# Optimization experiments

Measured on AMD Instinct MI355X. Metric: run time of the kernel, lower is better.

The kernel has to match this reference:

```python
import math
import jax, jax.numpy as jnp
import numpy as np

K, B, T = 6, 8, 12
DIM = 256
DH = 64          # dim_head
NH = 8           # num_heads
G = 8            # offset_groups
INNER = DH * NH  # 512
HALF = INNER // 2  # 256
OFF_D = INNER // G  # 64
HBEV = WBEV = 256
PW = PH = 102.4   # x/y range extents
SCALE = DH ** -0.5
OFF_SCALE = 4.0


def setup_inputs() -> dict:
    key = jax.random.key(0)
    ks = jax.random.split(key, 20)
    w = lambda i, shape: jax.random.normal(ks[i], shape, jnp.float32) * 0.05
    return {
        "dec_embed": jax.random.normal(ks[0], (K, B, T, DIM), jnp.float32),
        "bev_feat": jax.random.normal(ks[1], (B, DIM, HBEV, WBEV), jnp.float32),
        "query_scale": jax.random.uniform(ks[2], (K, B, T, HALF), jnp.float32),
        "ref_points": (jax.random.uniform(ks[3], (K, B, T, 2), jnp.float32) * 2.0 - 1.0) * 51.2,
        "Wq": w(4, (DIM, HALF)), "bq": jnp.zeros((HALF,), jnp.float32),
        "Wk": w(5, (DIM, HALF)),
        "Wv": w(6, (DIM, HALF)),
        "pq_W1": w(7, (HALF, HALF)), "pq_b1": jnp.zeros((HALF,), jnp.float32),
        "pq_W2": w(8, (HALF, HALF)), "pq_b2": jnp.zeros((HALF,), jnp.float32),
        "pk_W1": w(9, (HALF, HALF)), "pk_b1": jnp.zeros((HALF,), jnp.float32),
        "pk_W2": w(10, (HALF, HALF)), "pk_b2": jnp.zeros((HALF,), jnp.float32),
        "off_W1": w(11, (OFF_D // 2, OFF_D)), "off_b1": jnp.zeros((OFF_D,), jnp.float32),
        "off_W2": w(12, (OFF_D, 2)), "off_b2": jnp.zeros((2,), jnp.float32),
        "out_W": w(13, (HALF, DIM)), "out_b": jnp.zeros((DIM,), jnp.float32),
    }


def _grid_sample(im, grid):
    """F.grid_sample, bilinear, padding_mode='zeros', align_corners=False.
    im: (B,C,H,W), grid: (B,Hg,Wg,2) with (x,y) in [-1,1]. Returns (B,C,Hg,Wg)."""
    Bn, C, Hh, Ww = im.shape
    gx, gy = grid[..., 0], grid[..., 1]
    ix = ((gx + 1.0) * Ww - 1.0) * 0.5
    iy = ((gy + 1.0) * Hh - 1.0) * 0.5
    ix0 = jnp.floor(ix)
    iy0 = jnp.floor(iy)
    wx = (ix - ix0)[:, None]  # (B,1,Hg,Wg)
    wy = (iy - iy0)[:, None]
    imf = im.reshape(Bn, C, Hh * Ww)

    def gather(xq, yq):
        valid = (xq >= 0) & (xq < Ww) & (yq >= 0) & (yq < Hh)
        idx = (jnp.clip(yq, 0, Hh - 1) * Ww + jnp.clip(xq, 0, Ww - 1)).astype(jnp.int32)
        v = jnp.take_along_axis(imf, idx.reshape(Bn, 1, -1), axis=2)
        v = v.reshape(Bn, C, *xq.shape[1:])
        return v * valid[:, None].astype(im.dtype)

    v00 = gather(ix0, iy0)
    v01 = gather(ix0 + 1, iy0)
    v10 = gather(ix0, iy0 + 1)
    v11 = gather(ix0 + 1, iy0 + 1)
    return (v00 * (1 - wx) * (1 - wy) + v01 * wx * (1 - wy)
            + v10 * (1 - wx) * wy + v11 * wx * wy)


def _sine_embed(pos, hidden=256, temp=40.0):
    """DAB-DETR style sine embedding for 2D positions. pos: (...,2) -> (...,hidden)."""
    half = hidden // 2
    dim_t = jnp.arange(half, dtype=pos.dtype)
    dim_t = temp ** (2.0 * jnp.floor(dim_t / 2.0) / half)
    sc = 2.0 * math.pi
    ex = pos[..., 0, None] * sc / dim_t
    ey = pos[..., 1, None] * sc / dim_t

    def interleave(e):
        return jnp.stack((jnp.sin(e[..., 0::2]), jnp.cos(e[..., 1::2])), axis=-1).reshape(*e.shape[:-1], -1)

    return jnp.concatenate((interleave(ey), interleave(ex)), axis=-1)


def reference(dec_embed, bev_feat, query_scale, ref_points,
              Wq, bq, Wk, Wv,
              pq_W1, pq_b1, pq_W2, pq_b2,
              pk_W1, pk_b1, pk_W2, pk_b2,
              off_W1, off_b1, off_W2, off_b2,
              out_W, out_b):
    de = dec_embed.transpose(1, 0, 2, 3)     # (B,K,T,D)
    qs = query_scale.transpose(1, 0, 2, 3)   # (B,K,T,256)
    rp = ref_points.transpose(1, 0, 2, 3)    # (B,K,T,2)
    Bn, Kn, Tn = de.shape[:3]

    con_q = de @ Wq + bq                                    # (B,K,T,256)
    oin = con_q.reshape(Bn, Kn, Tn, G, OFF_D // 2)          # (B,K,T,G,32)
    off = jax.nn.gelu(oin @ off_W1 + off_b1, approximate=False)
    off = jnp.tanh(off @ off_W2 + off_b2) * OFF_SCALE       # (B,K,T,G,2)

    vgrid = rp[..., None, :] + off                          # (B,K,T,G,2)
    vgrid = vgrid.reshape(Bn, Kn * Tn, G, 2)
    norm = jnp.array([2.0 / PW, 2.0 / PH], vgrid.dtype)
    vgrid_scaled = vgrid * norm                             # ref_from_Q normalization

    con_k_map = jnp.einsum('bchw,cd->bdhw', bev_feat, Wk)   # 1x1 conv, no bias
    v_map = jnp.einsum('bchw,cd->bdhw', bev_feat, Wv)
    con_k = _grid_sample(con_k_map, vgrid_scaled)           # (B,256,KT,G)
    v = _grid_sample(v_map, vgrid_scaled)                   # (B,256,KT,G)

    ref_scaled = rp * norm                                  # (B,K,T,2)
    qse = _sine_embed(ref_scaled)                           # (B,K,T,256)
    pos_q = (jax.nn.relu(qse @ pq_W1 + pq_b1) @ pq_W2 + pq_b2) * qs
    kse = _sine_embed(vgrid_scaled)                         # (B,KT,G,256)
    pos_k = jax.nn.relu(kse @ pk_W1 + pk_b1) @ pk_W2 + pk_b2

    BS = Bn * Kn * Tn
    dh = HALF // NH  # 32 per-head content dim
    cq = con_q.reshape(BS, 1, NH, dh)
    pq = pos_q.reshape(BS, 1, NH, dh)
    ck = con_k.transpose(0, 2, 3, 1).reshape(BS, G, NH, dh)
    pk = pos_k.reshape(BS, G, NH, dh)
    vv = v.transpose(0, 2, 3, 1).reshape(BS, G, NH, dh)

    q = jnp.concatenate([cq, pq], -1).transpose(0, 2, 1, 3) * SCALE  # (BS,NH,1,64)
    k = jnp.concatenate([ck, pk], -1).transpose(0, 2, 1, 3)          # (BS,NH,G,64)
    vv = vv.transpose(0, 2, 1, 3)                                    # (BS,NH,G,32)

    sim = jnp.einsum('bhid,bhjd->bhij', q, k)               # (BS,NH,1,G)
    attn = jax.nn.softmax(sim, axis=-1)
    out = jnp.einsum('bhij,bhjd->bhid', attn, vv)           # (BS,NH,1,32)

    out = out.transpose(0, 2, 1, 3).reshape(Bn, Kn, Tn, HALF).transpose(1, 0, 2, 3)
    out = out @ out_W + out_b                               # (K,B,T,D)
    return dec_embed + out
```

## Files before the change

kernel.cpp:

```cpp
#include <hip/hip_runtime.h>
#include <math.h>

#define NK 6
#define NB 8
#define NT 12
#define D 256
#define DP (D+4)
#define NG 8
#define NHD 8
#define HW 256
#define NQ (NK*NB*NT)

__global__ __launch_bounds__(256)
void dca_kernel(const float* __restrict__ dec_embed,
                const float* __restrict__ bev_feat,
                const float* __restrict__ query_scale,
                const float* __restrict__ ref_points,
                const float* __restrict__ Wq,     const float* __restrict__ bq,
                const float* __restrict__ Wk,     const float* __restrict__ Wv,
                const float* __restrict__ pq_W1,  const float* __restrict__ pq_b1,
                const float* __restrict__ pq_W2,  const float* __restrict__ pq_b2,
                const float* __restrict__ pk_W1,  const float* __restrict__ pk_b1,
                const float* __restrict__ pk_W2,  const float* __restrict__ pk_b2,
                const float* __restrict__ off_W1, const float* __restrict__ off_b1,
                const float* __restrict__ off_W2, const float* __restrict__ off_b2,
                const float* __restrict__ out_W,  const float* __restrict__ out_b,
                float* __restrict__ out)
{
    __shared__ float de[D];
    __shared__ float conq[D];
    __shared__ float qse[D];
    __shared__ float tmp1[D];
    __shared__ float posq[D];
    __shared__ float oatt[D];
    __shared__ float h1[NG][64];
    __shared__ float gxy[NG][2];
    __shared__ float sim[NHD][NG];
    __shared__ float psum[64][4];
    __shared__ float samp[NG][DP];
    __shared__ float kseW[NG][DP];
    __shared__ float tmpk[NG][DP];
    __shared__ float wqk [NHD][DP];
    __shared__ float wqpk[NHD][DP];

    const int tid = threadIdx.x;
    const int q   = blockIdx.x;
    const int bb  = (q / NT) % NB;

    const float NORM = 0.01953125f;
    const float TWO_PI = 6.28318530717958647692f;
    const float L2_40_OVER_64 = 5.32192809488736234787f / 64.0f;

    de[tid] = dec_embed[(size_t)q * D + tid];
    __syncthreads();

    {
        float acc = bq[tid];
        #pragma unroll 4
        for (int i = 0; i < D; i += 4) {
            float4 d4 = *(const float4*)&de[i];
            acc += d4.x * Wq[(i + 0) * D + tid];
            acc += d4.y * Wq[(i + 1) * D + tid];
            acc += d4.z * Wq[(i + 2) * D + tid];
            acc += d4.w * Wq[(i + 3) * D + tid];
        }
        conq[tid] = acc;
        float rx = ref_points[(size_t)q * 2 + 0] * NORM;
        float ry = ref_points[(size_t)q * 2 + 1] * NORM;
        float pos = (tid < 128) ? ry : rx;
        int m = (tid & 127) >> 1;
        float freq = TWO_PI / exp2f((float)m * L2_40_OVER_64);
        float e = pos * freq;
        qse[tid] = (tid & 1) ? __cosf(e) : __sinf(e);
    }
    __syncthreads();

    for (int idx = tid; idx < NG * 64; idx += 256) {
        int g = idx >> 6, j = idx & 63;
        float acc = off_b1[j];
        #pragma unroll
        for (int i = 0; i < 32; i += 4) {
            float4 c4 = *(const float4*)&conq[g * 32 + i];
            acc += c4.x * off_W1[(i + 0) * 64 + j];
            acc += c4.y * off_W1[(i + 1) * 64 + j];
            acc += c4.z * off_W1[(i + 2) * 64 + j];
            acc += c4.w * off_W1[(i + 3) * 64 + j];
        }
        h1[g][j] = 0.5f * acc * (1.0f + erff(acc * 0.70710678118654752440f));
    }
    __syncthreads();

    if (tid < NG * 2) {
        int g = tid >> 1, c = tid & 1;
        float acc = off_b2[c];
        #pragma unroll
        for (int j = 0; j < 64; j += 4) {
            float4 hh = *(const float4*)&h1[g][j];
            acc += hh.x * off_W2[(j + 0) * 2 + c];
            acc += hh.y * off_W2[(j + 1) * 2 + c];
            acc += hh.z * off_W2[(j + 2) * 2 + c];
            acc += hh.w * off_W2[(j + 3) * 2 + c];
        }
        float off = tanhf(acc) * 4.0f;
        float rp  = ref_points[(size_t)q * 2 + c];
        gxy[g][c] = (rp + off) * NORM;
    }
    __syncthreads();

    {
        const float* ch = bev_feat + ((size_t)bb * D + tid) * HW * HW;
        float v00[NG], v01[NG], v10[NG], v11[NG], wxA[NG], wyA[NG];
        #pragma unroll
        for (int g = 0; g < NG; ++g) {
            float gx = gxy[g][0], gy = gxy[g][1];
            float ix = ((gx + 1.0f) * HW - 1.0f) * 0.5f;
            float iy = ((gy + 1.0f) * HW - 1.0f) * 0.5f;
            float fx0 = floorf(ix), fy0 = floorf(iy);
            wxA[g] = ix - fx0; wyA[g] = iy - fy0;
            int x0 = (int)fx0, y0 = (int)fy0;
            bool xin0 = (x0 >= 0) && (x0 < HW);
            bool xin1 = (x0 + 1 >= 0) && (x0 + 1 < HW);
            bool yin0 = (y0 >= 0) && (y0 < HW);
            bool yin1 = (y0 + 1 >= 0) && (y0 + 1 < HW);
            v00[g] = (yin0 && xin0) ? ch[y0 * HW + x0]           : 0.f;
            v01[g] = (yin0 && xin1) ? ch[y0 * HW + x0 + 1]       : 0.f;
            v10[g] = (yin1 && xin0) ? ch[(y0 + 1) * HW + x0]     : 0.f;
            v11[g] = (yin1 && xin1) ? ch[(y0 + 1) * HW + x0 + 1] : 0.f;
        }
        {
            int m = (tid & 127) >> 1;
            float freq = TWO_PI / exp2f((float)m * L2_40_OVER_64);
            #pragma unroll
            for (int g = 0; g < NG; ++g) {
                float pos = (tid < 128) ? gxy[g][1] : gxy[g][0];
                float e = pos * freq;
                kseW[g][tid] = (tid & 1) ? __cosf(e) : __sinf(e);
            }
        }
        {
            float acc[NHD] = {0.f,0.f,0.f,0.f,0.f,0.f,0.f,0.f};
            const float* wkrow = Wk + (size_t)tid * D;
            #pragma unroll
            for (int c = 0; c < D; c += 4) {
                float4 w  = *(const float4*)&wkrow[c];
                float4 cq = *(const float4*)&conq[c];
                acc[c >> 5] += w.x * cq.x + w.y * cq.y + w.z * cq.z + w.w * cq.w;
            }
            #pragma unroll
            for (int h = 0; h < NHD; ++h) wqk[h][tid] = acc[h];
        }
        #pragma unroll
        for (int g = 0; g < NG; ++g) {
            float wx = wxA[g], wy = wyA[g];
            samp[g][tid] = v00[g] * (1.f - wx) * (1.f - wy) + v01[g] * wx * (1.f - wy)
                         + v10[g] * (1.f - wx) * wy         + v11[g] * wx * wy;
        }
    }
    __syncthreads();

    {
        float acc[NG + 1];
        float biask = pk_b1[tid];
        #pragma unroll
        for (int g = 0; g < NG; ++g) acc[g] = biask;
        acc[NG] = pq_b1[tid];
        #pragma unroll 2
        for (int i = 0; i < D; i += 4) {
            float k0 = pk_W1[(i + 0) * D + tid], k1 = pk_W1[(i + 1) * D + tid];
            float k2 = pk_W1[(i + 2) * D + tid], k3 = pk_W1[(i + 3) * D + tid];
            float q0 = pq_W1[(i + 0) * D + tid], q1 = pq_W1[(i + 1) * D + tid];
            float q2 = pq_W1[(i + 2) * D + tid], q3 = pq_W1[(i + 3) * D + tid];
            #pragma unroll
            for (int g = 0; g < NG; ++g) {
                float4 s = *(const float4*)&kseW[g][i];
                acc[g] += s.x * k0 + s.y * k1 + s.z * k2 + s.w * k3;
            }
            float4 t = *(const float4*)&qse[i];
            acc[NG] += t.x * q0 + t.y * q1 + t.z * q2 + t.w * q3;
        }
        #pragma unroll
        for (int g = 0; g < NG; ++g) tmpk[g][tid] = fmaxf(acc[g], 0.f);
        tmp1[tid] = fmaxf(acc[NG], 0.f);
    }
    __syncthreads();

    {
        float a2 = pq_b2[tid];
        #pragma unroll 4
        for (int i = 0; i < D; i += 4) {
            float4 t = *(const float4*)&tmp1[i];
            a2 += t.x * pq_W2[(i + 0) * D + tid];
            a2 += t.y * pq_W2[(i + 1) * D + tid];
            a2 += t.z * pq_W2[(i + 2) * D + tid];
            a2 += t.w * pq_W2[(i + 3) * D + tid];
        }
        posq[tid] = a2 * query_scale[(size_t)q * D + tid];
    }
    __syncthreads();

    {
        float acc[NHD] = {0.f,0.f,0.f,0.f,0.f,0.f,0.f,0.f};
        const float* wrow = pk_W2 + (size_t)tid * D;
        #pragma unroll
        for (int c = 0; c < D; c += 4) {
            float4 w  = *(const float4*)&wrow[c];
            float4 p4 = *(const float4*)&posq[c];
            acc[c >> 5] += w.x * p4.x + w.y * p4.y + w.z * p4.z + w.w * p4.w;
        }
        #pragma unroll
        for (int h = 0; h < NHD; ++h) wqpk[h][tid] = acc[h];
    }
    __syncthreads();

    {
        int pair = tid >> 2, part = tid & 3;
        int h = pair >> 3, g = pair & 7;
        int i0 = part * 64;
        float s = 0.f;
        #pragma unroll
        for (int i = i0; i < i0 + 64; i += 4) {
            float4 a = *(const float4*)&samp[g][i];
            float4 b = *(const float4*)&wqk[h][i];
            float4 c = *(const float4*)&tmpk[g][i];
            float4 d = *(const float4*)&wqpk[h][i];
            s += a.x * b.x + a.y * b.y + a.z * b.z + a.w * b.w;
            s += c.x * d.x + c.y * d.y + c.z * d.z + c.w * d.w;
        }
        psum[pair][part] = s;
    }
    __syncthreads();
    if (tid < 64) {
        float s = psum[tid][0] + psum[tid][1] + psum[tid][2] + psum[tid][3];
        sim[tid >> 3][tid & 7] = s * 0.125f;
    }
    __syncthreads();

    if (tid < NHD) {
        int h = tid;
        float mx = sim[h][0];
        for (int g = 1; g < NG; ++g) mx = fmaxf(mx, sim[h][g]);
        float ex[NG], sum = 0.f;
        #pragma unroll
        for (int g = 0; g < NG; ++g) { ex[g] = __expf(sim[h][g] - mx); sum += ex[g]; }
        float inv = 1.0f / sum;
        #pragma unroll
        for (int g = 0; g < NG; ++g) sim[h][g] = ex[g] * inv;
    }
    __syncthreads();

    {
        float wsm[NHD];
        #pragma unroll
        for (int h = 0; h < NHD; ++h) wsm[h] = 0.f;
        #pragma unroll
        for (int g = 0; g < NG; ++g) {
            float sv = samp[g][tid];
            #pragma unroll
            for (int h = 0; h < NHD; ++h) wsm[h] += sim[h][g] * sv;
        }
        #pragma unroll
        for (int h = 0; h < NHD; ++h) kseW[h][tid] = wsm[h];
    }
    __syncthreads();

    {
        int h = tid >> 5;
        float acc = 0.f;
        #pragma unroll 4
        for (int i = 0; i < D; i += 4) {
            float4 w4 = *(const float4*)&kseW[h][i];
            acc += w4.x * Wv[(i + 0) * D + tid];
            acc += w4.y * Wv[(i + 1) * D + tid];
            acc += w4.z * Wv[(i + 2) * D + tid];
            acc += w4.w * Wv[(i + 3) * D + tid];
        }
        oatt[tid] = acc;
    }
    __syncthreads();

    {
        float acc = out_b[tid];
        #pragma unroll 4
        for (int i = 0; i < D; i += 4) {
            float4 o4 = *(const float4*)&oatt[i];
            acc += o4.x * out_W[(i + 0) * D + tid];
            acc += o4.y * out_W[(i + 1) * D + tid];
            acc += o4.z * out_W[(i + 2) * D + tid];
            acc += o4.w * out_W[(i + 3) * D + tid];
        }
        out[(size_t)q * D + tid] = acc + de[tid];
    }
}

extern "C" void kernel_launch(void* const* d_in, const int* in_sizes, int n_in,
                              void* d_out, int out_size, void* d_ws, size_t ws_size,
                              hipStream_t stream) {
    const float* dec_embed   = (const float*)d_in[0];
    const float* bev_feat    = (const float*)d_in[1];
    const float* query_scale = (const float*)d_in[2];
    const float* ref_points  = (const float*)d_in[3];
    const float* Wq     = (const float*)d_in[4];
    const float* bq     = (const float*)d_in[5];
    const float* Wk     = (const float*)d_in[6];
    const float* Wv     = (const float*)d_in[7];
    const float* pq_W1  = (const float*)d_in[8];
    const float* pq_b1  = (const float*)d_in[9];
    const float* pq_W2  = (const float*)d_in[10];
    const float* pq_b2  = (const float*)d_in[11];
    const float* pk_W1  = (const float*)d_in[12];
    const float* pk_b1  = (const float*)d_in[13];
    const float* pk_W2  = (const float*)d_in[14];
    const float* pk_b2  = (const float*)d_in[15];
    const float* off_W1 = (const float*)d_in[16];
    const float* off_b1 = (const float*)d_in[17];
    const float* off_W2 = (const float*)d_in[18];
    const float* off_b2 = (const float*)d_in[19];
    const float* out_W  = (const float*)d_in[20];
    const float* out_b  = (const float*)d_in[21];
    float* out = (float*)d_out;

    dca_kernel<<<NQ, 256, 0, stream>>>(dec_embed, bev_feat, query_scale, ref_points,
                                       Wq, bq, Wk, Wv,
                                       pq_W1, pq_b1, pq_W2, pq_b2,
                                       pk_W1, pk_b1, pk_W2, pk_b2,
                                       off_W1, off_b1, off_W2, off_b2,
                                       out_W, out_b, out);
}
```

Measured before the change: 722.5 us.

## Process two queries per block to reuse weight loads across queries

Each block now handles a pair of queries instead of one, halving the grid to 288 blocks. Every weight matrix (Wq, Wk, pk/pq MLPs, Wv, out_W) is loaded once per block and applied to both queries, halving global weight traffic per query. In exchange, shared memory roughly doubles, register pressure rises (e.g. 18 accumulators in the positional MLP), and a 288-block grid may underfill the 256 CUs on MI355X.

```diff
diff --git a/kernel.cpp b/kernel.cpp
--- a/kernel.cpp
+++ b/kernel.cpp
@@ -10,285 +10,319 @@
 #define NHD 8
 #define HW 256
 #define NQ (NK*NB*NT)
+#define NBLK (NQ/2)
 
 __global__ __launch_bounds__(256)
-void dca_kernel(const float* __restrict__ dec_embed,
-                const float* __restrict__ bev_feat,
-                const float* __restrict__ query_scale,
-                const float* __restrict__ ref_points,
-                const float* __restrict__ Wq,     const float* __restrict__ bq,
-                const float* __restrict__ Wk,     const float* __restrict__ Wv,
-                const float* __restrict__ pq_W1,  const float* __restrict__ pq_b1,
-                const float* __restrict__ pq_W2,  const float* __restrict__ pq_b2,
-                const float* __restrict__ pk_W1,  const float* __restrict__ pk_b1,
-                const float* __restrict__ pk_W2,  const float* __restrict__ pk_b2,
-                const float* __restrict__ off_W1, const float* __restrict__ off_b1,
-                const float* __restrict__ off_W2, const float* __restrict__ off_b2,
-                const float* __restrict__ out_W,  const float* __restrict__ out_b,
-                float* __restrict__ out)
+void dca_pair(const float* __restrict__ dec_embed,
+              const float* __restrict__ bev_feat,
+              const float* __restrict__ query_scale,
+              const float* __restrict__ ref_points,
+              const float* __restrict__ Wq,     const float* __restrict__ bq,
+              const float* __restrict__ Wk,     const float* __restrict__ Wv,
+              const float* __restrict__ pq_W1,  const float* __restrict__ pq_b1,
+              const float* __restrict__ pq_W2,  const float* __restrict__ pq_b2,
+              const float* __restrict__ pk_W1,  const float* __restrict__ pk_b1,
+              const float* __restrict__ pk_W2,  const float* __restrict__ pk_b2,
+              const float* __restrict__ off_W1, const float* __restrict__ off_b1,
+              const float* __restrict__ off_W2, const float* __restrict__ off_b2,
+              const float* __restrict__ out_W,  const float* __restrict__ out_b,
+              float* __restrict__ out)
 {
-    __shared__ float de[D];
-    __shared__ float conq[D];
-    __shared__ float qse[D];
-    __shared__ float tmp1[D];
-    __shared__ float posq[D];
-    __shared__ float oatt[D];
-    __shared__ float h1[NG][64];
-    __shared__ float gxy[NG][2];
-    __shared__ float sim[NHD][NG];
-    __shared__ float psum[64][4];
-    __shared__ float samp[NG][DP];
-    __shared__ float kseW[NG][DP];
-    __shared__ float tmpk[NG][DP];
-    __shared__ float wqk [NHD][DP];
-    __shared__ float wqpk[NHD][DP];
+    __shared__ float de[2][D];
+    __shared__ float conq[2][D];
+    __shared__ float qse[2][D];
+    __shared__ float posq[2][D];
+    __shared__ float h1buf[2][NG*64];
+    __shared__ float gxy[2][NG][2];
+    __shared__ float sim[2][NHD][NG];
+    __shared__ float samp[2][NG][DP];
+    __shared__ float kst [2][NG][DP];
+    __shared__ float wqk [2][NHD][DP];
+    __shared__ float wqpk[2][NHD][DP];
 
     const int tid = threadIdx.x;
-    const int q   = blockIdx.x;
-    const int bb  = (q / NT) % NB;
+    const int q0  = blockIdx.x * 2;
+    const int bb  = (q0 / NT) % NB;
 
     const float NORM = 0.01953125f;
     const float TWO_PI = 6.28318530717958647692f;
     const float L2_40_OVER_64 = 5.32192809488736234787f / 64.0f;
 
-    de[tid] = dec_embed[(size_t)q * D + tid];
-    __syncthreads();
-
-    {
-        float acc = bq[tid];
+    de[0][tid] = dec_embed[(size_t)q0 * D + tid];
+    de[1][tid] = dec_embed[(size_t)(q0 + 1) * D + tid];
+    __syncthreads();
+
+    {
+        float a0 = bq[tid], a1 = a0;
         #pragma unroll 4
         for (int i = 0; i < D; i += 4) {
-            float4 d4 = *(const float4*)&de[i];
-            acc += d4.x * Wq[(i + 0) * D + tid];
-            acc += d4.y * Wq[(i + 1) * D + tid];
-            acc += d4.z * Wq[(i + 2) * D + tid];
-            acc += d4.w * Wq[(i + 3) * D + tid];
-        }
-        conq[tid] = acc;
-        float rx = ref_points[(size_t)q * 2 + 0] * NORM;
-        float ry = ref_points[(size_t)q * 2 + 1] * NORM;
-        float pos = (tid < 128) ? ry : rx;
+            float w0 = Wq[(i + 0) * D + tid], w1 = Wq[(i + 1) * D + tid];
+            float w2 = Wq[(i + 2) * D + tid], w3 = Wq[(i + 3) * D + tid];
+            float4 d0 = *(const float4*)&de[0][i];
+            float4 d1 = *(const float4*)&de[1][i];
+            a0 += d0.x * w0 + d0.y * w1 + d0.z * w2 + d0.w * w3;
+            a1 += d1.x * w0 + d1.y * w1 + d1.z * w2 + d1.w * w3;
+        }
+        conq[0][tid] = a0;
+        conq[1][tid] = a1;
         int m = (tid & 127) >> 1;
         float freq = TWO_PI / exp2f((float)m * L2_40_OVER_64);
-        float e = pos * freq;
-        qse[tid] = (tid & 1) ? __cosf(e) : __sinf(e);
+        #pragma unroll
+        for (int p = 0; p < 2; ++p) {
+            float rx = ref_points[(size_t)(q0 + p) * 2 + 0] * NORM;
+            float ry = ref_points[(size_t)(q0 + p) * 2 + 1] * NORM;
+            float pos = (tid < 128) ? ry : rx;
+            float e = pos * freq;
+            qse[p][tid] = (tid & 1) ? __cosf(e) : __sinf(e);
+        }
     }
     __syncthreads();
 
     for (int idx = tid; idx < NG * 64; idx += 256) {
         int g = idx >> 6, j = idx & 63;
-        float acc = off_b1[j];
+        float a0 = off_b1[j], a1 = a0;
         #pragma unroll
         for (int i = 0; i < 32; i += 4) {
-            float4 c4 = *(const float4*)&conq[g * 32 + i];
-            acc += c4.x * off_W1[(i + 0) * 64 + j];
-            acc += c4.y * off_W1[(i + 1) * 64 + j];
-            acc += c4.z * off_W1[(i + 2) * 64 + j];
-            acc += c4.w * off_W1[(i + 3) * 64 + j];
-        }
-        h1[g][j] = 0.5f * acc * (1.0f + erff(acc * 0.70710678118654752440f));
+            float w0 = off_W1[(i + 0) * 64 + j], w1 = off_W1[(i + 1) * 64 + j];
+            float w2 = off_W1[(i + 2) * 64 + j], w3 = off_W1[(i + 3) * 64 + j];
+            float4 c0 = *(const float4*)&conq[0][g * 32 + i];
+            float4 c1 = *(const float4*)&conq[1][g * 32 + i];
+            a0 += c0.x * w0 + c0.y * w1 + c0.z * w2 + c0.w * w3;
+            a1 += c1.x * w0 + c1.y * w1 + c1.z * w2 + c1.w * w3;
+        }
+        h1buf[0][idx] = 0.5f * a0 * (1.0f + erff(a0 * 0.70710678118654752440f));
+        h1buf[1][idx] = 0.5f * a1 * (1.0f + erff(a1 * 0.70710678118654752440f));
     }
     __syncthreads();
 
     if (tid < NG * 2) {
         int g = tid >> 1, c = tid & 1;
-        float acc = off_b2[c];
+        float a0 = off_b2[c], a1 = a0;
         #pragma unroll
         for (int j = 0; j < 64; j += 4) {
-            float4 hh = *(const float4*)&h1[g][j];
-            acc += hh.x * off_W2[(j + 0) * 2 + c];
-            acc += hh.y * off_W2[(j + 1) * 2 + c];
-            acc += hh.z * off_W2[(j + 2) * 2 + c];
-            acc += hh.w * off_W2[(j + 3) * 2 + c];
-        }
-        float off = tanhf(acc) * 4.0f;
-        float rp  = ref_points[(size_t)q * 2 + c];
-        gxy[g][c] = (rp + off) * NORM;
-    }
-    __syncthreads();
-
-    {
-        const float* ch = bev_feat + ((size_t)bb * D + tid) * HW * HW;
-        float v00[NG], v01[NG], v10[NG], v11[NG], wxA[NG], wyA[NG];
-        #pragma unroll
-        for (int g = 0; g < NG; ++g) {
-            float gx = gxy[g][0], gy = gxy[g][1];
-            float ix = ((gx + 1.0f) * HW - 1.0f) * 0.5f;
-            float iy = ((gy + 1.0f) * HW - 1.0f) * 0.5f;
-            float fx0 = floorf(ix), fy0 = floorf(iy);
-            wxA[g] = ix - fx0; wyA[g] = iy - fy0;
-            int x0 = (int)fx0, y0 = (int)fy0;
-            bool xin0 = (x0 >= 0) && (x0 < HW);
-            bool xin1 = (x0 + 1 >= 0) && (x0 + 1 < HW);
-            bool yin0 = (y0 >= 0) && (y0 < HW);
-            bool yin1 = (y0 + 1 >= 0) && (y0 + 1 < HW);
-            v00[g] = (yin0 && xin0) ? ch[y0 * HW + x0]           : 0.f;
-            v01[g] = (yin0 && xin1) ? ch[y0 * HW + x0 + 1]       : 0.f;
-            v10[g] = (yin1 && xin0) ? ch[(y0 + 1) * HW + x0]     : 0.f;
-            v11[g] = (yin1 && xin1) ? ch[(y0 + 1) * HW + x0 + 1] : 0.f;
+            float w0 = off_W2[(j + 0) * 2 + c], w1 = off_W2[(j + 1) * 2 + c];
+            float w2 = off_W2[(j + 2) * 2 + c], w3 = off_W2[(j + 3) * 2 + c];
+            float4 h0 = *(const float4*)&h1buf[0][g * 64 + j];
+            float4 h14 = *(const float4*)&h1buf[1][g * 64 + j];
+            a0 += h0.x * w0 + h0.y * w1 + h0.z * w2 + h0.w * w3;
+            a1 += h14.x * w0 + h14.y * w1 + h14.z * w2 + h14.w * w3;
+        }
+        gxy[0][g][c] = (ref_points[(size_t)q0 * 2 + c] + tanhf(a0) * 4.0f) * NORM;
+        gxy[1][g][c] = (ref_points[(size_t)(q0 + 1) * 2 + c] + tanhf(a1) * 4.0f) * NORM;
+    }
+    __syncthreads();
+
+    {
+        const float* ch = bev_feat + ((size_t)bb * D + tid) * (HW * HW);
+        int m = (tid & 127) >> 1;
+        float freq = TWO_PI / exp2f((float)m * L2_40_OVER_64);
+        #pragma unroll 1
+        for (int p = 0; p < 2; ++p) {
+            float v00[NG], v01[NG], v10[NG], v11[NG], wxA[NG], wyA[NG];
+            #pragma unroll
+            for (int g = 0; g < NG; ++g) {
+                float gx = gxy[p][g][0], gy = gxy[p][g][1];
+                float ix = ((gx + 1.0f) * HW - 1.0f) * 0.5f;
+                float iy = ((gy + 1.0f) * HW - 1.0f) * 0.5f;
+                float fx0 = floorf(ix), fy0 = floorf(iy);
+                wxA[g] = ix - fx0; wyA[g] = iy - fy0;
+                int x0 = (int)fx0, y0 = (int)fy0;
+                bool xin0 = (x0 >= 0) && (x0 < HW);
+                bool xin1 = (x0 + 1 >= 0) && (x0 + 1 < HW);
+                bool yin0 = (y0 >= 0) && (y0 < HW);
+                bool yin1 = (y0 + 1 >= 0) && (y0 + 1 < HW);
+                v00[g] = (yin0 && xin0) ? ch[y0 * HW + x0]           : 0.f;
+                v01[g] = (yin0 && xin1) ? ch[y0 * HW + x0 + 1]       : 0.f;
+                v10[g] = (yin1 && xin0) ? ch[(y0 + 1) * HW + x0]     : 0.f;
+                v11[g] = (yin1 && xin1) ? ch[(y0 + 1) * HW + x0 + 1] : 0.f;
+            }
+            #pragma unroll
+            for (int g = 0; g < NG; ++g) {
+                float pos = (tid < 128) ? gxy[p][g][1] : gxy[p][g][0];
+                float e = pos * freq;
+                kst[p][g][tid] = (tid & 1) ? __cosf(e) : __sinf(e);
+            }
+            #pragma unroll
+            for (int g = 0; g < NG; ++g) {
+                float wx = wxA[g], wy = wyA[g];
+                samp[p][g][tid] = v00[g] * (1.f - wx) * (1.f - wy) + v01[g] * wx * (1.f - wy)
+                                + v10[g] * (1.f - wx) * wy         + v11[g] * wx * wy;
+            }
         }
         {
-            int m = (tid & 127) >> 1;
-            float freq = TWO_PI / exp2f((float)m * L2_40_OVER_64);
-            #pragma unroll
-            for (int g = 0; g < NG; ++g) {
-                float pos = (tid < 128) ? gxy[g][1] : gxy[g][0];
-                float e = pos * freq;
-                kseW[g][tid] = (tid & 1) ? __cosf(e) : __sinf(e);
-            }
-        }
-        {
-            float acc[NHD] = {0.f,0.f,0.f,0.f,0.f,0.f,0.f,0.f};
+            float ak[2][NHD] = {{0.f}};
             const float* wkrow = Wk + (size_t)tid * D;
             #pragma unroll
             for (int c = 0; c < D; c += 4) {
                 float4 w  = *(const float4*)&wkrow[c];
-                float4 cq = *(const float4*)&conq[c];
-                acc[c >> 5] += w.x * cq.x + w.y * cq.y + w.z * cq.z + w.w * cq.w;
-            }
-            #pragma unroll
-            for (int h = 0; h < NHD; ++h) wqk[h][tid] = acc[h];
-        }
-        #pragma unroll
-        for (int g = 0; g < NG; ++g) {
-            float wx = wxA[g], wy = wyA[g];
-            samp[g][tid] = v00[g] * (1.f - wx) * (1.f - wy) + v01[g] * wx * (1.f - wy)
-                         + v10[g] * (1.f - wx) * wy         + v11[g] * wx * wy;
-        }
-    }
-    __syncthreads();
-
-    {
-        float acc[NG + 1];
-        float biask = pk_b1[tid];
-        #pragma unroll
-        for (int g = 0; g < NG; ++g) acc[g] = biask;
-        acc[NG] = pq_b1[tid];
+                float4 c0 = *(const float4*)&conq[0][c];
+                float4 c1 = *(const float4*)&conq[1][c];
+                ak[0][c >> 5] += w.x * c0.x + w.y * c0.y + w.z * c0.z + w.w * c0.w;
+                ak[1][c >> 5] += w.x * c1.x + w.y * c1.y + w.z * c1.z + w.w * c1.w;
+            }
+            #pragma unroll
+            for (int h = 0; h < NHD; ++h) {
+                wqk[0][h][tid] = ak[0][h];
+                wqk[1][h][tid] = ak[1][h];
+            }
+        }
+    }
+    __syncthreads();
+
+    {
+        float acc[2][NG + 1];
+        float bk = pk_b1[tid], bqv = pq_b1[tid];
+        #pragma unroll
+        for (int p = 0; p < 2; ++p) {
+            #pragma unroll
+            for (int g = 0; g < NG; ++g) acc[p][g] = bk;
+            acc[p][NG] = bqv;
+        }
         #pragma unroll 2
         for (int i = 0; i < D; i += 4) {
             float k0 = pk_W1[(i + 0) * D + tid], k1 = pk_W1[(i + 1) * D + tid];
             float k2 = pk_W1[(i + 2) * D + tid], k3 = pk_W1[(i + 3) * D + tid];
-            float q0 = pq_W1[(i + 0) * D + tid], q1 = pq_W1[(i + 1) * D + tid];
-            float q2 = pq_W1[(i + 2) * D + tid], q3 = pq_W1[(i + 3) * D + tid];
-            #pragma unroll
-            for (int g = 0; g < NG; ++g) {
-                float4 s = *(const float4*)&kseW[g][i];
-                acc[g] += s.x * k0 + s.y * k1 + s.z * k2 + s.w * k3;
-            }
-            float4 t = *(const float4*)&qse[i];
-            acc[NG] += t.x * q0 + t.y * q1 + t.z * q2 + t.w * q3;
-        }
-        #pragma unroll
-        for (int g = 0; g < NG; ++g) tmpk[g][tid] = fmaxf(acc[g], 0.f);
-        tmp1[tid] = fmaxf(acc[NG], 0.f);
-    }
-    __syncthreads();
-
-    {
-        float a2 = pq_b2[tid];
+            float u0 = pq_W1[(i + 0) * D + tid], u1 = pq_W1[(i + 1) * D + tid];
+            float u2 = pq_W1[(i + 2) * D + tid], u3 = pq_W1[(i + 3) * D + tid];
+            #pragma unroll
+            for (int p = 0; p < 2; ++p) {
+                #pragma unroll
+                for (int g = 0; g < NG; ++g) {
+                    float4 s = *(const float4*)&kst[p][g][i];
+                    acc[p][g] += s.x * k0 + s.y * k1 + s.z * k2 + s.w * k3;
+                }
+                float4 t = *(const float4*)&qse[p][i];
+                acc[p][NG] += t.x * u0 + t.y * u1 + t.z * u2 + t.w * u3;
+            }
+        }
+        __syncthreads();
+        #pragma unroll
+        for (int p = 0; p < 2; ++p) {
+            #pragma unroll
+            for (int g = 0; g < NG; ++g) kst[p][g][tid] = fmaxf(acc[p][g], 0.f);
+            h1buf[p][tid] = fmaxf(acc[p][NG], 0.f);
+        }
+    }
+    __syncthreads();
+
+    {
+        float a0 = pq_b2[tid], a1 = a0;
         #pragma unroll 4
         for (int i = 0; i < D; i += 4) {
-            float4 t = *(const float4*)&tmp1[i];
-            a2 += t.x * pq_W2[(i + 0) * D + tid];
-            a2 += t.y * pq_W2[(i + 1) * D + tid];
-            a2 += t.z * pq_W2[(i + 2) * D + tid];
-            a2 += t.w * pq_W2[(i + 3) * D + tid];
-        }
-        posq[tid] = a2 * query_scale[(size_t)q * D + tid];
-    }
-    __syncthreads();
-
-    {
-        float acc[NHD] = {0.f,0.f,0.f,0.f,0.f,0.f,0.f,0.f};
+            float w0 = pq_W2[(i + 0) * D + tid], w1 = pq_W2[(i + 1) * D + tid];
+            float w2 = pq_W2[(i + 2) * D + tid], w3 = pq_W2[(i + 3) * D + tid];
+            float4 t0 = *(const float4*)&h1buf[0][i];
+            float4 t1 = *(const float4*)&h1buf[1][i];
+            a0 += t0.x * w0 + t0.y * w1 + t0.z * w2 + t0.w * w3;
+            a1 += t1.x * w0 + t1.y * w1 + t1.z * w2 + t1.w * w3;
+        }
+        posq[0][tid] = a0 * query_scale[(size_t)q0 * D + tid];
+        posq[1][tid] = a1 * query_scale[(size_t)(q0 + 1) * D + tid];
+    }
+    __syncthreads();
+
+    {
+        float aw[2][NHD] = {{0.f}};
         const float* wrow = pk_W2 + (size_t)tid * D;
         #pragma unroll
         for (int c = 0; c < D; c += 4) {
             float4 w  = *(const float4*)&wrow[c];
-            float4 p4 = *(const float4*)&posq[c];
-            acc[c >> 5] += w.x * p4.x + w.y * p4.y + w.z * p4.z + w.w * p4.w;
-        }
-        #pragma unroll
-        for (int h = 0; h < NHD; ++h) wqpk[h][tid] = acc[h];
-    }
-    __syncthreads();
-
-    {
-        int pair = tid >> 2, part = tid & 3;
-        int h = pair >> 3, g = pair & 7;
-        int i0 = part * 64;
+            float4 p0 = *(const float4*)&posq[0][c];
+            float4 p1 = *(const float4*)&posq[1][c];
+            aw[0][c >> 5] += w.x * p0.x + w.y * p0.y + w.z * p0.z + w.w * p0.w;
+            aw[1][c >> 5] += w.x * p1.x + w.y * p1.y + w.z * p1.z + w.w * p1.w;
+        }
+        #pragma unroll
+        for (int h = 0; h < NHD; ++h) {
+            wqpk[0][h][tid] = aw[0][h];
+            wqpk[1][h][tid] = aw[1][h];
+        }
+    }
+    __syncthreads();
+
+    {
+        int p = tid >> 7;
+        int rem = tid & 127;
+        int h = rem >> 4;
+        int g = (rem >> 1) & 7;
+        int i0 = (tid & 1) * 128;
         float s = 0.f;
         #pragma unroll
-        for (int i = i0; i < i0 + 64; i += 4) {
-            float4 a = *(const float4*)&samp[g][i];
-            float4 b = *(const float4*)&wqk[h][i];
-            float4 c = *(const float4*)&tmpk[g][i];
-            float4 d = *(const float4*)&wqpk[h][i];
+        for (int i = i0; i < i0 + 128; i += 4) {
+            float4 a = *(const float4*)&samp[p][g][i];
+            float4 b = *(const float4*)&wqk[p][h][i];
+            float4 c = *(const float4*)&kst[p][g][i];
+            float4 d = *(const float4*)&wqpk[p][h][i];
             s += a.x * b.x + a.y * b.y + a.z * b.z + a.w * b.w;
             s += c.x * d.x + c.y * d.y + c.z * d.z + c.w * d.w;
         }
-        psum[pair][part] = s;
-    }
-    __syncthreads();
-    if (tid < 64) {
-        float s = psum[tid][0] + psum[tid][1] + psum[tid][2] + psum[tid][3];
-        sim[tid >> 3][tid & 7] = s * 0.125f;
-    }
-    __syncthreads();
-
-    if (tid < NHD) {
-        int h = tid;
-        float mx = sim[h][0];
-        for (int g = 1; g < NG; ++g) mx = fmaxf(mx, sim[h][g]);
+        s += __shfl_down(s, 1, 64);
+        if (!(tid & 1)) sim[p][h][g] = s * 0.125f;
+    }
+    __syncthreads();
+
+    if (tid < 2 * NHD) {
+        int p = tid >> 3, h = tid & 7;
+        float mx = sim[p][h][0];
+        for (int g = 1; g < NG; ++g) mx = fmaxf(mx, sim[p][h][g]);
         float ex[NG], sum = 0.f;
         #pragma unroll
-        for (int g = 0; g < NG; ++g) { ex[g] = __expf(sim[h][g] - mx); sum += ex[g]; }
+        for (int g = 0; g < NG; ++g) { ex[g] = __expf(sim[p][h][g] - mx); sum += ex[g]; }
         float inv = 1.0f / sum;
         #pragma unroll
-        for (int g = 0; g < NG; ++g) sim[h][g] = ex[g] * inv;
-    }
-    __syncthreads();
-
-    {
-        float wsm[NHD];
-        #pragma unroll
-        for (int h = 0; h < NHD; ++h) wsm[h] = 0.f;
-        #pragma unroll
-        for (int g = 0; g < NG; ++g) {
-            float sv = samp[g][tid];
-            #pragma unroll
-            for (int h = 0; h < NHD; ++h) wsm[h] += sim[h][g] * sv;
-        }
-        #pragma unroll
-        for (int h = 0; h < NHD; ++h) kseW[h][tid] = wsm[h];
+        for (int g = 0; g < NG; ++g) sim[p][h][g] = ex[g] * inv;
+    }
+    __syncthreads();
+
+    {
+        #pragma unroll
+        for (int p = 0; p < 2; ++p) {
+            float wsm[NHD];
+            #pragma unroll
+            for (int h = 0; h < NHD; ++h) wsm[h] = 0.f;
+            #pragma unroll
+            for (int g = 0; g < NG; ++g) {
+                float sv = samp[p][g][tid];
+                #pragma unroll
+                for (int h = 0; h < NHD; ++h) wsm[h] += sim[p][h][g] * sv;
+            }
+            #pragma unroll
+            for (int h = 0; h < NHD; ++h) kst[p][h][tid] = wsm[h];
+        }
     }
     __syncthreads();
 
     {
         int h = tid >> 5;
-        float acc = 0.f;
+        float a0 = 0.f, a1 = 0.f;
         #pragma unroll 4
         for (int i = 0; i < D; i += 4) {
-            float4 w4 = *(const float4*)&kseW[h][i];
-            acc += w4.x * Wv[(i + 0) * D + tid];
-            acc += w4.y * Wv[(i + 1) * D + tid];
-            acc += w4.z * Wv[(i + 2) * D + tid];
-            acc += w4.w * Wv[(i + 3) * D + tid];
-        }
-        oatt[tid] = acc;
-    }
-    __syncthreads();
-
-    {
-        float acc = out_b[tid];
+            float w0 = Wv[(i + 0) * D + tid], w1 = Wv[(i + 1) * D + tid];
+            float w2 = Wv[(i + 2) * D + tid], w3 = Wv[(i + 3) * D + tid];
+            float4 k0 = *(const float4*)&kst[0][h][i];
+            float4 k1 = *(const float4*)&kst[1][h][i];
+            a0 += k0.x * w0 + k0.y * w1 + k0.z * w2 + k0.w * w3;
+            a1 += k1.x * w0 + k1.y * w1 + k1.z * w2 + k1.w * w3;
+        }
+        qse[0][tid] = a0;
+        qse[1][tid] = a1;
+    }
+    __syncthreads();
+
+    {
+        float b = out_b[tid];
+        float a0 = b, a1 = b;
         #pragma unroll 4
         for (int i = 0; i < D; i += 4) {
-            float4 o4 = *(const float4*)&oatt[i];
-            acc += o4.x * out_W[(i + 0) * D + tid];
-            acc += o4.y * out_W[(i + 1) * D + tid];
-            acc += o4.z * out_W[(i + 2) * D + tid];
-            acc += o4.w * out_W[(i + 3) * D + tid];
-        }
-        out[(size_t)q * D + tid] = acc + de[tid];
+            float w0 = out_W[(i + 0) * D + tid], w1 = out_W[(i + 1) * D + tid];
+            float w2 = out_W[(i + 2) * D + tid], w3 = out_W[(i + 3) * D + tid];
+            float4 o0 = *(const float4*)&qse[0][i];
+            float4 o1 = *(const float4*)&qse[1][i];
+            a0 += o0.x * w0 + o0.y * w1 + o0.z * w2 + o0.w * w3;
+            a1 += o1.x * w0 + o1.y * w1 + o1.z * w2 + o1.w * w3;
+        }
+        out[(size_t)q0 * D + tid]       = a0 + de[0][tid];
+        out[(size_t)(q0 + 1) * D + tid] = a1 + de[1][tid];
     }
 }
 
@@ -319,7 +353,7 @@
     const float* out_b  = (const float*)d_in[21];
     float* out = (float*)d_out;
 
-    dca_kernel<<<NQ, 256, 0, stream>>>(dec_embed, bev_feat, query_scale, ref_points,
+    dca_pair<<<NBLK, 256, 0, stream>>>(dec_embed, bev_feat, query_scale, ref_points,
                                        Wq, bq, Wk, Wv,
                                        pq_W1, pq_b1, pq_W2, pq_b2,
                                        pk_W1, pk_b1, pk_W2, pk_b2,
```

Measured after the change: 744.1 us. +3.0%, slower.
